# Optimization experiments

Measured on AMD Instinct MI355X. Metric: run time of the kernel, lower is better.

Reference implementation:

```python
import jax, jax.numpy as jnp
import numpy as np

B, T, DQ, DK, DV, H = 4, 2048, 1024, 1024, 1024, 16
HD = DV // H  # head dim = 64


def setup_inputs() -> dict:
    key = jax.random.key(0)
    ks = jax.random.split(key, 12)
    def xavier(k, fan_out, fan_in):
        std = (2.0 / (fan_in + fan_out)) ** 0.5
        return jax.random.normal(k, (fan_out, fan_in), dtype=jnp.float32) * std
    return {
        "q": jax.random.normal(ks[0], (B, T, DQ), dtype=jnp.float32),
        "k": jax.random.normal(ks[1], (B, T, DK), dtype=jnp.float32),
        "v": jax.random.normal(ks[2], (B, T, DV), dtype=jnp.float32),
        "mask": jnp.ones((B, T), dtype=jnp.int32),
        "Wq": xavier(ks[3], DV, DQ), "bq": jnp.zeros((DV,), jnp.float32),
        "Wk": xavier(ks[4], DV, DK), "bk": jnp.zeros((DV,), jnp.float32),
        "Wv": xavier(ks[5], DV, DV), "bv": jnp.zeros((DV,), jnp.float32),
        "Wo": xavier(ks[6], DV, DV), "bo": jnp.zeros((DV,), jnp.float32),
    }


def reference(q, k, v, mask, Wq, bq, Wk, bk, Wv, bv, Wo, bo):
    # Linear projections (torch Linear: x @ W.T + b)
    qp = q @ Wq.T + bq  # (B,T,DV)
    kp = k @ Wk.T + bk
    vp = v @ Wv.T + bv
    # split into heads: torch's split(dim=-1)+cat(dim=0) == reshape to (B,T,H,HD) then move H out
    qh = qp.reshape(B, T, H, HD).transpose(0, 2, 1, 3)  # (B,H,T,HD)
    kh = kp.reshape(B, T, H, HD).transpose(0, 2, 1, 3)
    vh = vp.reshape(B, T, H, HD).transpose(0, 2, 1, 3)
    # NOTE: original scales by 1/sqrt(dim_v) (full dim), not 1/sqrt(head_dim)
    scores = jnp.einsum("bhsd,bhtd->bhst", qh, kh) / jnp.sqrt(jnp.float32(DV))
    scores = jnp.where(mask[:, None, None, :] == 0, jnp.float32(-65504.0), scores)
    attn = jax.nn.softmax(scores, axis=-1)  # dropout disabled (p=0 / eval)
    o = jnp.einsum("bhst,bhtd->bhsd", attn, vh)  # (B,H,T,HD)
    o = o.transpose(0, 2, 1, 3).reshape(B, T, DV)
    return o @ Wo.T + bo
```

## Files before the change

kernel.cpp:

```cpp
#include <hip/hip_runtime.h>
#include <cstdint>
#include <cstddef>


typedef __attribute__((ext_vector_type(8))) short bf16x8;
typedef __attribute__((ext_vector_type(4))) short bf16x4;
typedef __attribute__((ext_vector_type(4))) float f32x4;
typedef __attribute__((ext_vector_type(16))) float f32x16;
typedef __attribute__((ext_vector_type(4))) unsigned uint4v;

#define MFMA16(a, b, c) __builtin_amdgcn_mfma_f32_16x16x32_bf16((a), (b), (c), 0, 0, 0)
#define MFMA32(a, b, c) __builtin_amdgcn_mfma_f32_32x32x16_bf16((a), (b), (c), 0, 0, 0)

__device__ __forceinline__ void gload_lds16(const void* g, void* l) {
  __builtin_amdgcn_global_load_lds((const __attribute__((address_space(1))) void*)g,
                                   (__attribute__((address_space(3))) void*)l,
                                   16, 0, 0);
}

__device__ __forceinline__ unsigned short f2bf(float f) {
  union { float f; unsigned u; } x; x.f = f;
  unsigned r = x.u + 0x7fffu + ((x.u >> 16) & 1u);
  return (unsigned short)(r >> 16);
}

__device__ __forceinline__ unsigned cvtpk(float lo, float hi) {
  unsigned r;
  asm("v_cvt_pk_bf16_f32 %0, %1, %2" : "=v"(r) : "v"(lo), "v"(hi));
  return r;
}

__device__ __forceinline__ unsigned short f2bf_cvt(float f) {
  unsigned r;
  asm("v_cvt_pk_bf16_f32 %0, %1, 0" : "=v"(r) : "v"(f));
  return (unsigned short)r;
}

__device__ __forceinline__ float fexp2(float x) {
#if __has_builtin(__builtin_amdgcn_exp2f)
  return __builtin_amdgcn_exp2f(x);
#else
  return exp2f(x);
#endif
}

struct CvtArgs {
  const float* src[7];
  unsigned short* dst[7];
};

__global__ __launch_bounds__(256) void cvt_kernel(CvtArgs a) {
  const int bid = blockIdx.x;
  int t, i;
  if (bid < 24576) { t = bid >> 13; i = ((bid & 8191) << 8) + threadIdx.x; }
  else { const int r = bid - 24576; t = 3 + (r >> 10); i = ((r & 1023) << 8) + threadIdx.x; }
  const float4 v = ((const float4*)a.src[t])[i];
  ushort4 o;
  o.x = f2bf(v.x); o.y = f2bf(v.y); o.z = f2bf(v.z); o.w = f2bf(v.w);
  ((ushort4*)a.dst[t])[i] = o;
}

__global__ __launch_bounds__(256) void mask_kernel(const int* __restrict__ m,
                                                   float* __restrict__ mf) {
  const int i = blockIdx.x * 256 + threadIdx.x;
  mf[i] = m[i] ? 0.0f : -65504.0f;
}

struct GemmB {
  const unsigned short* A[3];
  const unsigned short* W[3];
  const float* bias[3];
  unsigned short* out[3];
};

template <int NB, int F32OUT>
__global__ __launch_bounds__(256, 2) void gemm_nt(GemmB gb, float* fout) {
  constexpr int K = 1024, N = 1024;
  __shared__ unsigned short As[128 * 32];
  __shared__ unsigned short Bs[128 * 32];

  const int nwg = NB * 512;
  const int wg = blockIdx.x;
  const int swz = (wg & 7) * (nwg >> 3) + (wg >> 3);
  const int which = swz >> 9;
  const int rr = swz & 511;
  const int m0 = (rr >> 3) * 128, n0 = (rr & 7) * 128;

  const unsigned short* __restrict__ A = gb.A[which];
  const unsigned short* __restrict__ W = gb.W[which];
  const float* __restrict__ bias = gb.bias[which];

  const int tid = threadIdx.x;
  const int w = tid >> 6, l = tid & 63;
  const int wm = (w >> 1) * 64, wn = (w & 1) * 64;
  const int fr = l & 15, kg = (l >> 4) * 8;

  const int srow = w * 32 + (l >> 2);
  const int sk = (l & 3) * 8;
  const unsigned short* Ag0 = A + (size_t)(m0 + srow) * K + sk;
  const unsigned short* Ag1 = Ag0 + (size_t)16 * K;
  const unsigned short* Wg0 = W + (size_t)(n0 + srow) * K + sk;
  const unsigned short* Wg1 = Wg0 + (size_t)16 * K;
  unsigned short* Asl0 = As + w * 1024;
  unsigned short* Asl1 = As + w * 1024 + 512;
  unsigned short* Bsl0 = Bs + w * 1024;
  unsigned short* Bsl1 = Bs + w * 1024 + 512;

  f32x4 acc[4][4] = {};

  for (int kt = 0; kt < K; kt += 32) {
    gload_lds16(Ag0 + kt, Asl0);
    gload_lds16(Ag1 + kt, Asl1);
    gload_lds16(Wg0 + kt, Bsl0);
    gload_lds16(Wg1 + kt, Bsl1);
    __syncthreads();

    bf16x8 af[4], bfv[4];
#pragma unroll
    for (int mt = 0; mt < 4; ++mt)
      af[mt] = *(const bf16x8*)(As + (wm + mt * 16 + fr) * 32 + kg);
#pragma unroll
    for (int nt = 0; nt < 4; ++nt)
      bfv[nt] = *(const bf16x8*)(Bs + (wn + nt * 16 + fr) * 32 + kg);
#pragma unroll
    for (int mt = 0; mt < 4; ++mt)
#pragma unroll
      for (int nt = 0; nt < 4; ++nt)
        acc[mt][nt] = MFMA16(af[mt], bfv[nt], acc[mt][nt]);
    __syncthreads();
  }

  const int rg = (l >> 4) * 4;
  float bv[4];
#pragma unroll
  for (int nt = 0; nt < 4; ++nt) bv[nt] = bias[n0 + wn + nt * 16 + fr];

#pragma unroll
  for (int mt = 0; mt < 4; ++mt) {
#pragma unroll
    for (int nt = 0; nt < 4; ++nt) {
      const int col = n0 + wn + nt * 16 + fr;
#pragma unroll
      for (int r = 0; r < 4; ++r) {
        const size_t row = (size_t)(m0 + wm + mt * 16 + rg + r);
        const float vv = acc[mt][nt][r] + bv[nt];
        if (F32OUT) fout[row * N + col] = vv;
        else        gb.out[which][row * N + col] = f2bf(vv);
      }
    }
  }
}

__global__ __launch_bounds__(256, 3) void attn_kernel(
    const unsigned short* __restrict__ QP,
    const unsigned short* __restrict__ KP,
    const unsigned short* __restrict__ VP,
    const float* __restrict__ maskf,
    unsigned short* __restrict__ O)
{
  __shared__ unsigned short Kls[64 * 64];
  __shared__ unsigned short VTls[64 * 64];
  __shared__ float wscr[4][32];

  const int wg = blockIdx.x;
  const int swz = (wg & 7) * 128 + (wg >> 3);
  const int qt = swz & 15, h = (swz >> 4) & 15, b = swz >> 8;

  const int tid = threadIdx.x, w = tid >> 6, l = tid & 63;
  const int lq = l & 31, hi = l >> 5, hi8 = hi * 8;
  const size_t brow = (size_t)b * 2048;
  const int hcol = h * 64;
  const int q0 = qt * 128 + w * 32;

  bf16x8 qf[4];
  {
    const unsigned short* qp = QP + (brow + q0 + lq) * 1024 + hcol + hi8;
    qf[0] = *(const bf16x8*)(qp);
    qf[1] = *(const bf16x8*)(qp + 16);
    qf[2] = *(const bf16x8*)(qp + 32);
    qf[3] = *(const bf16x8*)(qp + 48);
  }

  const int skv = l >> 3;
  const int schunk = 8 * ((l & 7) ^ skv);
  const unsigned short* Ksrc0 = KP + (brow + w * 16 + skv) * 1024 + hcol + schunk;
  const unsigned short* Ksrc1 = Ksrc0 + (size_t)8 * 1024;
  unsigned short* Kdst0 = Kls + (w * 2 + 0) * 512;
  unsigned short* Kdst1 = Kls + (w * 2 + 1) * 512;

  const int tkv = (l & 15) * 4;
  const int td = w * 16 + (l >> 4) * 4;
  const unsigned short* Vsrc = VP + (brow + tkv) * 1024 + hcol + td;

  float m_run = -3e38f, l_run = 0.f;
  f32x16 ob0 = {}, ob1 = {};
  const float cs = 0.04508422823f;
  const float* mrow = maskf + (size_t)b * 2048;
  const int dsw = (lq & 7) << 4;
  const char* vtb0 = (const char*)VTls + (size_t)lq * 128;
  const char* vtb1 = (const char*)VTls + (size_t)(32 + lq) * 128;
  const char* klb0 = (const char*)Kls + (size_t)lq * 128;
  const char* klb1 = (const char*)Kls + (size_t)(32 + lq) * 128;

  for (int kv0 = 0; kv0 < 2048; kv0 += 64) {
    __syncthreads();
    gload_lds16(Ksrc0 + (size_t)kv0 * 1024, Kdst0);
    gload_lds16(Ksrc1 + (size_t)kv0 * 1024, Kdst1);
    {
      const unsigned short* vs = Vsrc + (size_t)kv0 * 1024;
      ushort4 r0 = *(const ushort4*)(vs);
      ushort4 r1 = *(const ushort4*)(vs + 1024);
      ushort4 r2 = *(const ushort4*)(vs + 2048);
      ushort4 r3 = *(const ushort4*)(vs + 3072);
      ushort4 c0 = {r0.x, r1.x, r2.x, r3.x};
      ushort4 c1 = {r0.y, r1.y, r2.y, r3.y};
      ushort4 c2 = {r0.z, r1.z, r2.z, r3.z};
      ushort4 c3 = {r0.w, r1.w, r2.w, r3.w};
      char* vb = (char*)VTls;
      *(ushort4*)(vb + (td + 0) * 128 + ((tkv * 2) ^ (((td + 0) & 7) << 4))) = c0;
      *(ushort4*)(vb + (td + 1) * 128 + ((tkv * 2) ^ (((td + 1) & 7) << 4))) = c1;
      *(ushort4*)(vb + (td + 2) * 128 + ((tkv * 2) ^ (((td + 2) & 7) << 4))) = c2;
      *(ushort4*)(vb + (td + 3) * 128 + ((tkv * 2) ^ (((td + 3) & 7) << 4))) = c3;
    }
    __syncthreads();

    f32x16 s0 = {}, s1 = {};
#pragma unroll
    for (int s = 0; s < 4; ++s) {
      const int co = (s * 32 + hi * 16) ^ dsw;
      bf16x8 k0 = *(const bf16x8*)(klb0 + co);
      bf16x8 k1 = *(const bf16x8*)(klb1 + co);
      s0 = MFMA32(k0, qf[s], s0);
      s1 = MFMA32(k1, qf[s], s1);
    }

    const float mfv = mrow[kv0 + l];
    if (__any(mfv != 0.0f)) {
#pragma unroll
      for (int r = 0; r < 16; ++r) {
        const int kvr = (r & 3) + 8 * (r >> 2) + 4 * hi;
        s0[r] += 32.0f * mrow[kv0 + kvr];
        s1[r] += 32.0f * mrow[kv0 + 32 + kvr];
      }
    }

    float t0[8];
#pragma unroll
    for (int r = 0; r < 8; ++r) t0[r] = fmaxf(s0[r], s0[r + 8]);
#pragma unroll
    for (int r = 0; r < 8; ++r) t0[r] = fmaxf(t0[r], fmaxf(s1[r], s1[r + 8]));
#pragma unroll
    for (int r = 0; r < 4; ++r) t0[r] = fmaxf(t0[r], t0[r + 4]);
    float mx = fmaxf(fmaxf(t0[0], t0[1]), fmaxf(t0[2], t0[3]));
    mx = fmaxf(mx, __shfl_xor(mx, 32));

    if (!__all(mx - m_run <= 256.0f)) {
      const float mn = fmaxf(m_run, mx);
      const float alpha = fexp2((m_run - mn) * cs);
      if (l < 32) wscr[w][lq] = alpha;
      m_run = mn;
      l_run *= alpha;
#pragma unroll
      for (int g = 0; g < 4; ++g) {
        const f32x4 av = *(const f32x4*)&wscr[w][g * 8 + hi * 4];
#pragma unroll
        for (int c = 0; c < 4; ++c) {
          ob0[g * 4 + c] *= av[c];
          ob1[g * 4 + c] *= av[c];
        }
      }
    }

    const float m2 = m_run * cs;
    float ps0 = 0.f, ps1 = 0.f, ps2 = 0.f, ps3 = 0.f;
#pragma unroll
    for (int r = 0; r < 16; r += 4) {
      s0[r + 0] = fexp2(fmaf(s0[r + 0], cs, -m2)); ps0 += s0[r + 0];
      s0[r + 1] = fexp2(fmaf(s0[r + 1], cs, -m2)); ps1 += s0[r + 1];
      s0[r + 2] = fexp2(fmaf(s0[r + 2], cs, -m2)); ps2 += s0[r + 2];
      s0[r + 3] = fexp2(fmaf(s0[r + 3], cs, -m2)); ps3 += s0[r + 3];
    }
#pragma unroll
    for (int r = 0; r < 16; r += 4) {
      s1[r + 0] = fexp2(fmaf(s1[r + 0], cs, -m2)); ps0 += s1[r + 0];
      s1[r + 1] = fexp2(fmaf(s1[r + 1], cs, -m2)); ps1 += s1[r + 1];
      s1[r + 2] = fexp2(fmaf(s1[r + 2], cs, -m2)); ps2 += s1[r + 2];
      s1[r + 3] = fexp2(fmaf(s1[r + 3], cs, -m2)); ps3 += s1[r + 3];
    }
    float ps = (ps0 + ps1) + (ps2 + ps3);
    l_run += ps + __shfl_xor(ps, 32);

#define PV_BLOCK(SP, BK)                                                     \
  {                                                                          \
    _Pragma("unroll")                                                        \
    for (int t = 0; t < 2; ++t) {                                            \
      uint4v pw;                                                             \
      pw[0] = cvtpk(SP[8 * t + 0], SP[8 * t + 1]);                           \
      pw[1] = cvtpk(SP[8 * t + 2], SP[8 * t + 3]);                           \
      pw[2] = cvtpk(SP[8 * t + 4], SP[8 * t + 5]);                           \
      pw[3] = cvtpk(SP[8 * t + 6], SP[8 * t + 7]);                           \
      const bf16x8 pa = __builtin_bit_cast(bf16x8, pw);                      \
      const int cA = ((BK) * 64 + t * 32 + hi8) ^ dsw;                       \
      const int cB = ((BK) * 64 + t * 32 + 16 + hi8) ^ dsw;                  \
      const bf16x4 va0 = *(const bf16x4*)(vtb0 + cA);                        \
      const bf16x4 vb0v = *(const bf16x4*)(vtb0 + cB);                       \
      const bf16x4 va1 = *(const bf16x4*)(vtb1 + cA);                        \
      const bf16x4 vb1v = *(const bf16x4*)(vtb1 + cB);                       \
      const bf16x8 v0 = {va0[0], va0[1], va0[2], va0[3],                     \
                         vb0v[0], vb0v[1], vb0v[2], vb0v[3]};                \
      const bf16x8 v1 = {va1[0], va1[1], va1[2], va1[3],                     \
                         vb1v[0], vb1v[1], vb1v[2], vb1v[3]};                \
      ob0 = MFMA32(pa, v0, ob0);                                             \
      ob1 = MFMA32(pa, v1, ob1);                                             \
    }                                                                        \
  }
    PV_BLOCK(s0, 0)
    PV_BLOCK(s1, 1)
#undef PV_BLOCK
  }

  if (l < 32) wscr[w][lq] = 1.0f / l_run;
#pragma unroll
  for (int g = 0; g < 4; ++g) {
    const f32x4 iv = *(const f32x4*)&wscr[w][g * 8 + hi * 4];
#pragma unroll
    for (int c = 0; c < 4; ++c) {
      const int qr = g * 8 + hi * 4 + c;
      const size_t row = brow + (size_t)(q0 + qr);
      O[row * 1024 + hcol + lq]      = f2bf_cvt(ob0[g * 4 + c] * iv[c]);
      O[row * 1024 + hcol + 32 + lq] = f2bf_cvt(ob1[g * 4 + c] * iv[c]);
    }
  }
}

extern "C" void kernel_launch(void* const* d_in, const int* in_sizes, int n_in,
                              void* d_out, int out_size, void* d_ws, size_t ws_size,
                              hipStream_t stream) {
  const float* q  = (const float*)d_in[0];
  const float* k  = (const float*)d_in[1];
  const float* v  = (const float*)d_in[2];
  const int*  msk = (const int*)d_in[3];
  const float* Wq = (const float*)d_in[4];
  const float* bq = (const float*)d_in[5];
  const float* Wk = (const float*)d_in[6];
  const float* bk = (const float*)d_in[7];
  const float* Wv = (const float*)d_in[8];
  const float* bv = (const float*)d_in[9];
  const float* Wo = (const float*)d_in[10];
  const float* bo = (const float*)d_in[11];

  char* ws = (char*)d_ws;
  const size_t SZ_BT = (size_t)8192 * 1024 * 2;
  const size_t SZ_W  = (size_t)1024 * 1024 * 2;
  unsigned short* qb  = (unsigned short*)(ws);
  unsigned short* kb  = (unsigned short*)(ws + SZ_BT);
  unsigned short* vb  = (unsigned short*)(ws + 2 * SZ_BT);
  unsigned short* Wqb = (unsigned short*)(ws + 3 * SZ_BT);
  unsigned short* Wkb = (unsigned short*)(ws + 3 * SZ_BT + SZ_W);
  unsigned short* Wvb = (unsigned short*)(ws + 3 * SZ_BT + 2 * SZ_W);
  unsigned short* Wob = (unsigned short*)(ws + 3 * SZ_BT + 3 * SZ_W);
  unsigned short* QPp = (unsigned short*)(ws + 3 * SZ_BT + 4 * SZ_W);
  unsigned short* KPp = (unsigned short*)(ws + 4 * SZ_BT + 4 * SZ_W);
  unsigned short* VPp = (unsigned short*)(ws + 5 * SZ_BT + 4 * SZ_W);
  unsigned short* AOp = (unsigned short*)(ws + 6 * SZ_BT + 4 * SZ_W);
  float*          mkf = (float*)(ws + 7 * SZ_BT + 4 * SZ_W);

  CvtArgs ca;
  ca.src[0] = q;  ca.dst[0] = qb;
  ca.src[1] = k;  ca.dst[1] = kb;
  ca.src[2] = v;  ca.dst[2] = vb;
  ca.src[3] = Wq; ca.dst[3] = Wqb;
  ca.src[4] = Wk; ca.dst[4] = Wkb;
  ca.src[5] = Wv; ca.dst[5] = Wvb;
  ca.src[6] = Wo; ca.dst[6] = Wob;
  cvt_kernel<<<dim3(28672), 256, 0, stream>>>(ca);
  mask_kernel<<<dim3(32), 256, 0, stream>>>(msk, mkf);

  GemmB g3;
  g3.A[0] = qb; g3.W[0] = Wqb; g3.bias[0] = bq; g3.out[0] = QPp;
  g3.A[1] = kb; g3.W[1] = Wkb; g3.bias[1] = bk; g3.out[1] = KPp;
  g3.A[2] = vb; g3.W[2] = Wvb; g3.bias[2] = bv; g3.out[2] = VPp;
  gemm_nt<3, 0><<<dim3(1536), 256, 0, stream>>>(g3, nullptr);

  attn_kernel<<<dim3(1024), 256, 0, stream>>>(QPp, KPp, VPp, mkf, AOp);

  GemmB g1;
  g1.A[0] = AOp; g1.W[0] = Wob; g1.bias[0] = bo; g1.out[0] = nullptr;
  gemm_nt<1, 1><<<dim3(512), 256, 0, stream>>>(g1, (float*)d_out);
}
```

Measured before the change: 404.9 us.

## Double-buffer LDS tiles in GEMM and attention kernels to overlap loads

Adds ping-pong LDS buffers to both the projection GEMM and the attention kernel, so the next K/V or A/W tile is fetched while the current tile feeds MFMAs. The attention kernel holds the next V rows in registers and writes the transposed tile to the spare buffer after the PV step. Each loop iteration drops to one barrier. In exchange, LDS use per block doubles and register pressure rises, which can lower occupancy. There is also some risk in relying on a single barrier to order async global_load_lds writes against reads of the other buffer.

```diff
diff --git a/kernel.cpp b/kernel.cpp
--- a/kernel.cpp
+++ b/kernel.cpp
@@ -76,8 +76,8 @@
 template <int NB, int F32OUT>
 __global__ __launch_bounds__(256, 2) void gemm_nt(GemmB gb, float* fout) {
   constexpr int K = 1024, N = 1024;
-  __shared__ unsigned short As[128 * 32];
-  __shared__ unsigned short Bs[128 * 32];
+  __shared__ unsigned short As[2][128 * 32];
+  __shared__ unsigned short Bs[2][128 * 32];
 
   const int nwg = NB * 512;
   const int wg = blockIdx.x;
@@ -101,32 +101,38 @@
   const unsigned short* Ag1 = Ag0 + (size_t)16 * K;
   const unsigned short* Wg0 = W + (size_t)(n0 + srow) * K + sk;
   const unsigned short* Wg1 = Wg0 + (size_t)16 * K;
-  unsigned short* Asl0 = As + w * 1024;
-  unsigned short* Asl1 = As + w * 1024 + 512;
-  unsigned short* Bsl0 = Bs + w * 1024;
-  unsigned short* Bsl1 = Bs + w * 1024 + 512;
+  const int sl0 = w * 1024, sl1 = w * 1024 + 512;
+
+  gload_lds16(Ag0, &As[0][sl0]);
+  gload_lds16(Ag1, &As[0][sl1]);
+  gload_lds16(Wg0, &Bs[0][sl0]);
+  gload_lds16(Wg1, &Bs[0][sl1]);
+  __syncthreads();
 
   f32x4 acc[4][4] = {};
 
   for (int kt = 0; kt < K; kt += 32) {
-    gload_lds16(Ag0 + kt, Asl0);
-    gload_lds16(Ag1 + kt, Asl1);
-    gload_lds16(Wg0 + kt, Bsl0);
-    gload_lds16(Wg1 + kt, Bsl1);
-    __syncthreads();
+    const int cur = (kt >> 5) & 1, nxt = cur ^ 1;
+    if (kt + 32 < K) {
+      gload_lds16(Ag0 + kt + 32, &As[nxt][sl0]);
+      gload_lds16(Ag1 + kt + 32, &As[nxt][sl1]);
+      gload_lds16(Wg0 + kt + 32, &Bs[nxt][sl0]);
+      gload_lds16(Wg1 + kt + 32, &Bs[nxt][sl1]);
+    }
 
     bf16x8 af[4], bfv[4];
 #pragma unroll
     for (int mt = 0; mt < 4; ++mt)
-      af[mt] = *(const bf16x8*)(As + (wm + mt * 16 + fr) * 32 + kg);
+      af[mt] = *(const bf16x8*)(&As[cur][(wm + mt * 16 + fr) * 32 + kg]);
 #pragma unroll
     for (int nt = 0; nt < 4; ++nt)
-      bfv[nt] = *(const bf16x8*)(Bs + (wn + nt * 16 + fr) * 32 + kg);
+      bfv[nt] = *(const bf16x8*)(&Bs[cur][(wn + nt * 16 + fr) * 32 + kg]);
 #pragma unroll
     for (int mt = 0; mt < 4; ++mt)
 #pragma unroll
       for (int nt = 0; nt < 4; ++nt)
         acc[mt][nt] = MFMA16(af[mt], bfv[nt], acc[mt][nt]);
+
     __syncthreads();
   }
 
@@ -158,8 +164,8 @@
     const float* __restrict__ maskf,
     unsigned short* __restrict__ O)
 {
-  __shared__ unsigned short Kls[64 * 64];
-  __shared__ unsigned short VTls[64 * 64];
+  __shared__ unsigned short Kls[2][64 * 64];
+  __shared__ unsigned short VTls[2][64 * 64];
   __shared__ float wscr[4][32];
 
   const int wg = blockIdx.x;
@@ -185,44 +191,64 @@
   const int schunk = 8 * ((l & 7) ^ skv);
   const unsigned short* Ksrc0 = KP + (brow + w * 16 + skv) * 1024 + hcol + schunk;
   const unsigned short* Ksrc1 = Ksrc0 + (size_t)8 * 1024;
-  unsigned short* Kdst0 = Kls + (w * 2 + 0) * 512;
-  unsigned short* Kdst1 = Kls + (w * 2 + 1) * 512;
+  const int kdst0 = (w * 2 + 0) * 512;
+  const int kdst1 = (w * 2 + 1) * 512;
 
   const int tkv = (l & 15) * 4;
   const int td = w * 16 + (l >> 4) * 4;
   const unsigned short* Vsrc = VP + (brow + tkv) * 1024 + hcol + td;
+  const int vco0 = (td + 0) * 128 + ((tkv * 2) ^ (((td + 0) & 7) << 4));
+  const int vco1 = (td + 1) * 128 + ((tkv * 2) ^ (((td + 1) & 7) << 4));
+  const int vco2 = (td + 2) * 128 + ((tkv * 2) ^ (((td + 2) & 7) << 4));
+  const int vco3 = (td + 3) * 128 + ((tkv * 2) ^ (((td + 3) & 7) << 4));
+
+  gload_lds16(Ksrc0, &Kls[0][kdst0]);
+  gload_lds16(Ksrc1, &Kls[0][kdst1]);
+  {
+    ushort4 r0 = *(const ushort4*)(Vsrc);
+    ushort4 r1 = *(const ushort4*)(Vsrc + 1024);
+    ushort4 r2 = *(const ushort4*)(Vsrc + 2048);
+    ushort4 r3 = *(const ushort4*)(Vsrc + 3072);
+    char* vb = (char*)&VTls[0][0];
+    ushort4 c0 = {r0.x, r1.x, r2.x, r3.x};
+    ushort4 c1 = {r0.y, r1.y, r2.y, r3.y};
+    ushort4 c2 = {r0.z, r1.z, r2.z, r3.z};
+    ushort4 c3 = {r0.w, r1.w, r2.w, r3.w};
+    *(ushort4*)(vb + vco0) = c0;
+    *(ushort4*)(vb + vco1) = c1;
+    *(ushort4*)(vb + vco2) = c2;
+    *(ushort4*)(vb + vco3) = c3;
+  }
+  __syncthreads();
 
   float m_run = -3e38f, l_run = 0.f;
   f32x16 ob0 = {}, ob1 = {};
   const float cs = 0.04508422823f;
   const float* mrow = maskf + (size_t)b * 2048;
   const int dsw = (lq & 7) << 4;
-  const char* vtb0 = (const char*)VTls + (size_t)lq * 128;
-  const char* vtb1 = (const char*)VTls + (size_t)(32 + lq) * 128;
-  const char* klb0 = (const char*)Kls + (size_t)lq * 128;
-  const char* klb1 = (const char*)Kls + (size_t)(32 + lq) * 128;
-
-  for (int kv0 = 0; kv0 < 2048; kv0 += 64) {
-    __syncthreads();
-    gload_lds16(Ksrc0 + (size_t)kv0 * 1024, Kdst0);
-    gload_lds16(Ksrc1 + (size_t)kv0 * 1024, Kdst1);
-    {
-      const unsigned short* vs = Vsrc + (size_t)kv0 * 1024;
-      ushort4 r0 = *(const ushort4*)(vs);
-      ushort4 r1 = *(const ushort4*)(vs + 1024);
-      ushort4 r2 = *(const ushort4*)(vs + 2048);
-      ushort4 r3 = *(const ushort4*)(vs + 3072);
-      ushort4 c0 = {r0.x, r1.x, r2.x, r3.x};
-      ushort4 c1 = {r0.y, r1.y, r2.y, r3.y};
-      ushort4 c2 = {r0.z, r1.z, r2.z, r3.z};
-      ushort4 c3 = {r0.w, r1.w, r2.w, r3.w};
-      char* vb = (char*)VTls;
-      *(ushort4*)(vb + (td + 0) * 128 + ((tkv * 2) ^ (((td + 0) & 7) << 4))) = c0;
-      *(ushort4*)(vb + (td + 1) * 128 + ((tkv * 2) ^ (((td + 1) & 7) << 4))) = c1;
-      *(ushort4*)(vb + (td + 2) * 128 + ((tkv * 2) ^ (((td + 2) & 7) << 4))) = c2;
-      *(ushort4*)(vb + (td + 3) * 128 + ((tkv * 2) ^ (((td + 3) & 7) << 4))) = c3;
-    }
-    __syncthreads();
+  const size_t rb0 = (size_t)lq * 128;
+  const size_t rb1 = (size_t)(32 + lq) * 128;
+
+  for (int it = 0; it < 32; ++it) {
+    const int cur = it & 1, nxt = cur ^ 1;
+    const int kv0 = it * 64;
+
+    ushort4 pr0, pr1, pr2, pr3;
+    if (it < 31) {
+      const size_t koff = (size_t)(kv0 + 64) * 1024;
+      gload_lds16(Ksrc0 + koff, &Kls[nxt][kdst0]);
+      gload_lds16(Ksrc1 + koff, &Kls[nxt][kdst1]);
+      const unsigned short* vs = Vsrc + koff;
+      pr0 = *(const ushort4*)(vs);
+      pr1 = *(const ushort4*)(vs + 1024);
+      pr2 = *(const ushort4*)(vs + 2048);
+      pr3 = *(const ushort4*)(vs + 3072);
+    }
+
+    const char* klb0 = (const char*)&Kls[cur][0] + rb0;
+    const char* klb1 = (const char*)&Kls[cur][0] + rb1;
+    const char* vtb0 = (const char*)&VTls[cur][0] + rb0;
+    const char* vtb1 = (const char*)&VTls[cur][0] + rb1;
 
     f32x16 s0 = {}, s1 = {};
 #pragma unroll
@@ -317,6 +343,20 @@
     PV_BLOCK(s0, 0)
     PV_BLOCK(s1, 1)
 #undef PV_BLOCK
+
+    if (it < 31) {
+      char* vb = (char*)&VTls[nxt][0];
+      ushort4 c0 = {pr0.x, pr1.x, pr2.x, pr3.x};
+      ushort4 c1 = {pr0.y, pr1.y, pr2.y, pr3.y};
+      ushort4 c2 = {pr0.z, pr1.z, pr2.z, pr3.z};
+      ushort4 c3 = {pr0.w, pr1.w, pr2.w, pr3.w};
+      *(ushort4*)(vb + vco0) = c0;
+      *(ushort4*)(vb + vco1) = c1;
+      *(ushort4*)(vb + vco2) = c2;
+      *(ushort4*)(vb + vco3) = c3;
+    }
+
+    __syncthreads();
   }
 
   if (l < 32) wscr[w][lq] = 1.0f / l_run;
```

After: 382.1 us. -5.6%, faster.
